# Kernel optimization log

Measured on AMD Instinct MI355X. Metric: run time of the kernel, lower is better.

## Reference

```python
import jax, jax.numpy as jnp
import numpy as np

E, K, D_IN, D_OUT, D_HID = 16, 2, 1024, 1024, 2048

def setup_inputs() -> dict:
    key = jax.random.key(0)
    ks = jax.random.split(key, 6)
    s_in = 1.0 / np.sqrt(D_IN)
    s_hid = 1.0 / np.sqrt(D_HID)
    return {
        "x": jax.random.normal(ks[0], (4096, D_IN), dtype=jnp.float32),
        "gate_w": jax.random.uniform(ks[1], (E, D_IN), jnp.float32, -s_in, s_in),
        "w1": jax.random.uniform(ks[2], (E, D_HID, D_IN), jnp.float32, -s_in, s_in),
        "b1": jax.random.uniform(ks[3], (E, D_HID), jnp.float32, -s_in, s_in),
        "w2": jax.random.uniform(ks[4], (E, D_OUT, D_HID), jnp.float32, -s_hid, s_hid),
        "b2": jax.random.uniform(ks[5], (E, D_OUT), jnp.float32, -s_hid, s_hid),
    }

def reference(x, gate_w, w1, b1, w2, b2):
    # gate: [B, E]
    gate_scores = jnp.einsum('bi,ei->be', x, gate_w)
    topk_vals, topk_idxs = jax.lax.top_k(gate_scores, K)  # [B, K]
    topk_weights = jax.nn.softmax(topk_vals, axis=-1)     # [B, K]
    # dense all-expert MLP (faithful to reference): [B, E, D_OUT]
    h = jax.nn.relu(jnp.einsum('bi,ehi->beh', x, w1) + b1[None])
    expert_outputs = jnp.einsum('beh,eoh->beo', h, w2) + b2[None]
    # gather selected experts: [B, K, D_OUT]
    sel = jnp.take_along_axis(expert_outputs, topk_idxs[:, :, None], axis=1)
    return jnp.sum(sel * topk_weights[:, :, None], axis=1)
```

## Files before the change

kernel.cpp:

```cpp
#include <hip/hip_runtime.h>
#include <hip/hip_bf16.h>
#include <math.h>

#define B_TOK 4096
#define NE 16
#define DI 1024
#define DH 2048
#define DOUT 1024
#define NSLOT (B_TOK * 2)

typedef unsigned short u16;
typedef short bfrag __attribute__((ext_vector_type(8)));
typedef float f32x4 __attribute__((ext_vector_type(4)));
typedef u16 u16x8 __attribute__((ext_vector_type(8)));

__device__ __forceinline__ u16 f2bf(float f) {
    union { float f; unsigned u; } v; v.f = f;
    return (u16)((v.u + 0x7fffu + ((v.u >> 16) & 1u)) >> 16);
}

__device__ __forceinline__ void async16(const void* g, void* lds) {
    __builtin_amdgcn_global_load_lds(
        (const __attribute__((address_space(1))) void*)g,
        (__attribute__((address_space(3))) void*)lds,
        16, 0, 0);
}

__global__ void zero_init(float* __restrict__ out, int n4) {
    int i = blockIdx.x * blockDim.x + threadIdx.x;
    if (i < n4) ((float4*)out)[i] = make_float4(0.f, 0.f, 0.f, 0.f);
}

__global__ void convert_bf16(const float* __restrict__ src, u16* __restrict__ dst, int n8) {
    int i = blockIdx.x * blockDim.x + threadIdx.x;
    if (i >= n8) return;
    const float4* s4 = (const float4*)src;
    float4 a = s4[2 * i], b = s4[2 * i + 1];
    u16x8 r;
    r[0] = f2bf(a.x); r[1] = f2bf(a.y); r[2] = f2bf(a.z); r[3] = f2bf(a.w);
    r[4] = f2bf(b.x); r[5] = f2bf(b.y); r[6] = f2bf(b.z); r[7] = f2bf(b.w);
    ((u16x8*)dst)[i] = r;
}

__global__ __launch_bounds__(256) void gate_topk(
    const float* __restrict__ x, const float* __restrict__ gw,
    int* __restrict__ token_e, float* __restrict__ token_w)
{
    int wave = threadIdx.x >> 6, lane = threadIdx.x & 63;
    int t = blockIdx.x * 4 + wave;
    const float4* x4 = (const float4*)(x + (size_t)t * DI);
    const float4* g4 = (const float4*)gw;
    double acc[NE];
#pragma unroll
    for (int e = 0; e < NE; ++e) acc[e] = 0.0;
#pragma unroll
    for (int i = 0; i < 4; ++i) {
        float4 xv = x4[lane + i * 64];
#pragma unroll
        for (int e = 0; e < NE; ++e) {
            float4 gv = g4[e * 256 + lane + i * 64];
            acc[e] += (double)xv.x * gv.x + (double)xv.y * gv.y
                    + (double)xv.z * gv.z + (double)xv.w * gv.w;
        }
    }
#pragma unroll
    for (int e = 0; e < NE; ++e) {
        double v = acc[e];
        for (int off = 32; off; off >>= 1) v += __shfl_xor(v, off, 64);
        acc[e] = v;
    }
    if (lane == 0) {
        int e0 = 0; double v0 = acc[0];
#pragma unroll
        for (int e = 1; e < NE; ++e) if (acc[e] > v0) { v0 = acc[e]; e0 = e; }
        int e1 = -1; double v1 = -1e300;
#pragma unroll
        for (int e = 0; e < NE; ++e) if (e != e0 && acc[e] > v1) { v1 = acc[e]; e1 = e; }
        float d = expf((float)(v1 - v0));
        float w0 = 1.f / (1.f + d);
        float w1 = d * w0;
        token_e[2 * t] = e0; token_e[2 * t + 1] = e1;
        token_w[2 * t] = w0; token_w[2 * t + 1] = w1;
    }
}

__global__ __launch_bounds__(1024) void route(
    const int* __restrict__ token_e, const float* __restrict__ token_w,
    int* __restrict__ counts, int* __restrict__ offsets,
    int* __restrict__ slot_token, float* __restrict__ slot_wgt)
{
    __shared__ int lcnt[NE];
    __shared__ int lcur[NE];
    int tid = threadIdx.x;
    if (tid < NE) lcnt[tid] = 0;
    __syncthreads();
    for (int i = tid; i < NSLOT; i += 1024) atomicAdd(&lcnt[token_e[i]], 1);
    __syncthreads();
    if (tid == 0) {
        int s = 0;
        for (int e = 0; e < NE; ++e) {
            int c = lcnt[e];
            counts[e] = c; offsets[e] = s; lcur[e] = s; s += c;
        }
    }
    __syncthreads();
    for (int i = tid; i < NSLOT; i += 1024) {
        int e = token_e[i];
        int pos = atomicAdd(&lcur[e], 1);
        slot_token[pos] = i >> 1;
        slot_wgt[pos] = token_w[i];
    }
}

template <int PHASE>
__global__ __launch_bounds__(256) void moe_gemm(
    const u16* __restrict__ Abuf,
    const u16* __restrict__ Bbuf,
    const float* __restrict__ bias,
    const int* __restrict__ counts, const int* __restrict__ offsets,
    const int* __restrict__ slot_token, const float* __restrict__ slot_wgt,
    u16* __restrict__ hb, float* __restrict__ out)
{
    constexpr int KDIM = (PHASE == 1) ? DI : DH;
    constexpr int NDIM = (PHASE == 1) ? DH : DOUT;

    const int e = blockIdx.z;
    const int cnt = counts[e];
    const int m0 = blockIdx.y * 128;
    if (m0 >= cnt) return;
    const int n0 = blockIdx.x * 128;
    const int sbase = offsets[e];

    __shared__ u16 ldsbuf[8192];
    u16* alds = ldsbuf;
    u16* blds = ldsbuf + 4096;

    const int tid = threadIdx.x;
    const int wv = tid >> 6, lane = tid & 63;
    const int lrow = lane >> 2, lkc = lane & 3;

    const int arow0 = wv * 16 + lrow;
    const int arow1 = 64 + wv * 16 + lrow;

    const u16* aptr0; const u16* aptr1;
    if (PHASE == 1) {
        int c = cnt - 1;
        int r0 = m0 + arow0; if (r0 > c) r0 = c;
        int r1 = m0 + arow1; if (r1 > c) r1 = c;
        aptr0 = Abuf + (size_t)slot_token[sbase + r0] * KDIM + lkc * 8;
        aptr1 = Abuf + (size_t)slot_token[sbase + r1] * KDIM + lkc * 8;
    } else {
        int s0 = sbase + m0 + arow0; if (s0 > NSLOT - 1) s0 = NSLOT - 1;
        int s1 = sbase + m0 + arow1; if (s1 > NSLOT - 1) s1 = NSLOT - 1;
        aptr0 = Abuf + (size_t)s0 * KDIM + lkc * 8;
        aptr1 = Abuf + (size_t)s1 * KDIM + lkc * 8;
    }
    const u16* bbase = Bbuf + (size_t)e * NDIM * KDIM;
    const u16* bptr0 = bbase + (size_t)(n0 + arow0) * KDIM + lkc * 8;
    const u16* bptr1 = bbase + (size_t)(n0 + arow1) * KDIM + lkc * 8;

    u16* alds_w0 = alds + wv * 512;
    u16* alds_w1 = alds + 2048 + wv * 512;
    u16* blds_w0 = blds + wv * 512;
    u16* blds_w1 = blds + 2048 + wv * 512;

    f32x4 acc[4][4];
#pragma unroll
    for (int i = 0; i < 4; ++i)
#pragma unroll
        for (int j = 0; j < 4; ++j) acc[i][j] = (f32x4){0.f, 0.f, 0.f, 0.f};

    const int wm = (wv & 1) * 64, wn = (wv >> 1) * 64;
    const int quad = lane >> 4, mr = lane & 15;
    const int aoff = (wm + mr) * 32 + quad * 8;
    const int boff = (wn + mr) * 32 + quad * 8;

    const int nk = KDIM / 32;
    for (int kt = 0; kt < nk; ++kt) {
        __syncthreads();
        async16(aptr0 + kt * 32, alds_w0);
        async16(aptr1 + kt * 32, alds_w1);
        async16(bptr0 + kt * 32, blds_w0);
        async16(bptr1 + kt * 32, blds_w1);
        __syncthreads();
        bfrag af[4], bf[4];
#pragma unroll
        for (int i = 0; i < 4; ++i) af[i] = *(const bfrag*)(alds + aoff + i * 512);
#pragma unroll
        for (int j = 0; j < 4; ++j) bf[j] = *(const bfrag*)(blds + boff + j * 512);
#pragma unroll
        for (int i = 0; i < 4; ++i)
#pragma unroll
            for (int j = 0; j < 4; ++j)
                acc[i][j] = __builtin_amdgcn_mfma_f32_16x16x32_bf16(af[i], bf[j], acc[i][j], 0, 0, 0);
    }

    const float* bias_e = bias + e * NDIM;
    if constexpr (PHASE == 1) {
#pragma unroll
        for (int i = 0; i < 4; ++i) {
            int mbase = wm + i * 16 + quad * 4;
#pragma unroll
            for (int j = 0; j < 4; ++j) {
                int n = n0 + wn + j * 16 + mr;
                float bv = bias_e[n];
#pragma unroll
                for (int r = 0; r < 4; ++r) {
                    int m = m0 + mbase + r;
                    if (m < cnt) {
                        float v = acc[i][j][r] + bv;
                        v = v > 0.f ? v : 0.f;
                        hb[(size_t)(sbase + m) * DH + n] = f2bf(v);
                    }
                }
            }
        }
    } else {
#pragma unroll
        for (int i = 0; i < 4; ++i) {
            int mbase = wm + i * 16 + quad * 4;
#pragma unroll
            for (int r = 0; r < 4; ++r) {
                int m = m0 + mbase + r;
                if (m < cnt) {
                    int slot = sbase + m;
                    int tok = slot_token[slot];
                    float wgt = slot_wgt[slot];
                    float* orow = out + (size_t)tok * DOUT + n0 + wn;
#pragma unroll
                    for (int j = 0; j < 4; ++j) {
                        int nl = j * 16 + mr;
                        float v = wgt * (acc[i][j][r] + bias_e[n0 + wn + nl]);
                        atomicAdd(orow + nl, v);
                    }
                }
            }
        }
    }
}

extern "C" void kernel_launch(void* const* d_in, const int* in_sizes, int n_in,
                              void* d_out, int out_size, void* d_ws, size_t ws_size,
                              hipStream_t stream) {
    const float* x  = (const float*)d_in[0];
    const float* gw = (const float*)d_in[1];
    const float* w1 = (const float*)d_in[2];
    const float* b1 = (const float*)d_in[3];
    const float* w2 = (const float*)d_in[4];
    const float* b2 = (const float*)d_in[5];
    float* out = (float*)d_out;

    char* ws = (char*)d_ws;
    u16* xb = (u16*)ws;
    u16* wb = (u16*)(ws + 8388608);
    u16* hb = (u16*)(ws + 8388608 + 67108864);
    char* rb = ws + 109051904;
    int*   counts     = (int*)(rb);
    int*   offsets    = (int*)(rb + 64);
    int*   token_e    = (int*)(rb + 192);
    float* token_w    = (float*)(rb + 192 + 32768);
    int*   slot_token = (int*)(rb + 192 + 65536);
    float* slot_wgt   = (float*)(rb + 192 + 98304);

    zero_init<<<4096, 256, 0, stream>>>(out, (B_TOK * DOUT) / 4);
    convert_bf16<<<2048, 256, 0, stream>>>(x, xb, (B_TOK * DI) / 8);
    convert_bf16<<<16384, 256, 0, stream>>>(w1, wb, (NE * DH * DI) / 8);
    gate_topk<<<1024, 256, 0, stream>>>(x, gw, token_e, token_w);
    route<<<1, 1024, 0, stream>>>(token_e, token_w, counts, offsets, slot_token, slot_wgt);
    moe_gemm<1><<<dim3(DH / 128, B_TOK / 128, NE), 256, 0, stream>>>(
        xb, wb, b1, counts, offsets, slot_token, slot_wgt, hb, out);
    convert_bf16<<<16384, 256, 0, stream>>>(w2, wb, (NE * DOUT * DH) / 8);
    moe_gemm<2><<<dim3(DOUT / 128, B_TOK / 128, NE), 256, 0, stream>>>(
        hb, wb, b2, counts, offsets, slot_token, slot_wgt, hb, out);
}
```

Before: 514.8 us.

## Double-buffer LDS tiles and remap MoE GEMM grid for XCD locality

```diff
diff --git a/kernel.cpp b/kernel.cpp
--- a/kernel.cpp
+++ b/kernel.cpp
@@ -123,17 +123,24 @@
 {
     constexpr int KDIM = (PHASE == 1) ? DI : DH;
     constexpr int NDIM = (PHASE == 1) ? DH : DOUT;
-
-    const int e = blockIdx.z;
+    constexpr int NT = NDIM / 128;
+    constexpr int MT = B_TOK / 128;
+    constexpr int PER_XCD = (NE * NT * MT) / 8;
+
+    const int id = blockIdx.x;
+    const int wg = (id & 7) * PER_XCD + (id >> 3);
+    const int e  = wg / (NT * MT);
+    const int rem = wg % (NT * MT);
+    const int nt = rem / MT;
+    const int mt = rem % MT;
+
     const int cnt = counts[e];
-    const int m0 = blockIdx.y * 128;
+    const int m0 = mt * 128;
     if (m0 >= cnt) return;
-    const int n0 = blockIdx.x * 128;
+    const int n0 = nt * 128;
     const int sbase = offsets[e];
 
-    __shared__ u16 ldsbuf[8192];
-    u16* alds = ldsbuf;
-    u16* blds = ldsbuf + 4096;
+    __shared__ u16 ldsbuf[2][8192];
 
     const int tid = threadIdx.x;
     const int wv = tid >> 6, lane = tid & 63;
@@ -159,11 +166,6 @@
     const u16* bptr0 = bbase + (size_t)(n0 + arow0) * KDIM + lkc * 8;
     const u16* bptr1 = bbase + (size_t)(n0 + arow1) * KDIM + lkc * 8;
 
-    u16* alds_w0 = alds + wv * 512;
-    u16* alds_w1 = alds + 2048 + wv * 512;
-    u16* blds_w0 = blds + wv * 512;
-    u16* blds_w1 = blds + 2048 + wv * 512;
-
     f32x4 acc[4][4];
 #pragma unroll
     for (int i = 0; i < 4; ++i)
@@ -176,13 +178,28 @@
     const int boff = (wn + mr) * 32 + quad * 8;
 
     const int nk = KDIM / 32;
+
+    {
+        u16* base = &ldsbuf[0][0];
+        async16(aptr0, base + wv * 512);
+        async16(aptr1, base + 2048 + wv * 512);
+        async16(bptr0, base + 4096 + wv * 512);
+        async16(bptr1, base + 4096 + 2048 + wv * 512);
+    }
+    __syncthreads();
+
     for (int kt = 0; kt < nk; ++kt) {
-        __syncthreads();
-        async16(aptr0 + kt * 32, alds_w0);
-        async16(aptr1 + kt * 32, alds_w1);
-        async16(bptr0 + kt * 32, blds_w0);
-        async16(bptr1 + kt * 32, blds_w1);
-        __syncthreads();
+        const int cur = kt & 1;
+        if (kt + 1 < nk) {
+            u16* base = &ldsbuf[cur ^ 1][0];
+            const int ko = (kt + 1) * 32;
+            async16(aptr0 + ko, base + wv * 512);
+            async16(aptr1 + ko, base + 2048 + wv * 512);
+            async16(bptr0 + ko, base + 4096 + wv * 512);
+            async16(bptr1 + ko, base + 4096 + 2048 + wv * 512);
+        }
+        const u16* alds = &ldsbuf[cur][0];
+        const u16* blds = alds + 4096;
         bfrag af[4], bf[4];
 #pragma unroll
         for (int i = 0; i < 4; ++i) af[i] = *(const bfrag*)(alds + aoff + i * 512);
@@ -193,6 +210,7 @@
 #pragma unroll
             for (int j = 0; j < 4; ++j)
                 acc[i][j] = __builtin_amdgcn_mfma_f32_16x16x32_bf16(af[i], bf[j], acc[i][j], 0, 0, 0);
+        __syncthreads();
     }
 
     const float* bias_e = bias + e * NDIM;
@@ -267,9 +285,9 @@
     convert_bf16<<<16384, 256, 0, stream>>>(w1, wb, (NE * DH * DI) / 8);
     gate_topk<<<1024, 256, 0, stream>>>(x, gw, token_e, token_w);
     route<<<1, 1024, 0, stream>>>(token_e, token_w, counts, offsets, slot_token, slot_wgt);
-    moe_gemm<1><<<dim3(DH / 128, B_TOK / 128, NE), 256, 0, stream>>>(
+    moe_gemm<1><<<NE * (DH / 128) * (B_TOK / 128), 256, 0, stream>>>(
         xb, wb, b1, counts, offsets, slot_token, slot_wgt, hb, out);
     convert_bf16<<<16384, 256, 0, stream>>>(w2, wb, (NE * DOUT * DH) / 8);
-    moe_gemm<2><<<dim3(DOUT / 128, B_TOK / 128, NE), 256, 0, stream>>>(
+    moe_gemm<2><<<NE * (DOUT / 128) * (B_TOK / 128), 256, 0, stream>>>(
         hb, wb, b2, counts, offsets, slot_token, slot_wgt, hb, out);
 }
```

Result: faster. 500.7 us (-2.7%).
